# Performance work log

Hardware: AMD Instinct MI355X
Metric: run time of the kernel (lower is better)

Reference implementation:

```python
import jax, jax.numpy as jnp
import numpy as np

S, D, H = 2048, 1024, 16
DH = D // H
EPS = 1e-5


def setup_inputs() -> dict:
    key = jax.random.key(0)
    ks = jax.random.split(key, 6)
    scale = 0.02
    return {
        "inputs": jax.random.normal(ks[0], (S, D), dtype=jnp.float32),
        "ln_w": jnp.ones((D,), dtype=jnp.float32),
        "ln_b": jnp.zeros((D,), dtype=jnp.float32),
        "Wq": jax.random.normal(ks[1], (D, D), dtype=jnp.float32) * scale,
        "Wk": jax.random.normal(ks[2], (D, D), dtype=jnp.float32) * scale,
        "Wv": jax.random.normal(ks[3], (D, D), dtype=jnp.float32) * scale,
        "Wo": jax.random.normal(ks[4], (D, D), dtype=jnp.float32) * scale,
    }


def reference(inputs, ln_w, ln_b, Wq, Wk, Wv, Wo):
    # Pre-LayerNorm (per token), matching eqx.nn.LayerNorm (eps=1e-5)
    mu = jnp.mean(inputs, axis=-1, keepdims=True)
    var = jnp.var(inputs, axis=-1, keepdims=True)
    x = (inputs - mu) / jnp.sqrt(var + EPS) * ln_w + ln_b  # [S, D]

    # QKV projections (eqx Linear: y = W @ x, no bias) -> [S, H, DH]
    q = (x @ Wq.T).reshape(S, H, DH)
    k = (x @ Wk.T).reshape(S, H, DH)
    v = (x @ Wv.T).reshape(S, H, DH)

    # Scaled dot-product attention; softmax forced to full precision
    scores = jnp.einsum("shd,thd->hst", q, k) / jnp.sqrt(jnp.asarray(DH, x.dtype))
    attn = jax.nn.softmax(scores.astype(jnp.float32), axis=-1).astype(x.dtype)
    # (dropout is identity in inference mode)
    ctx = jnp.einsum("hst,thd->shd", attn, v).reshape(S, D)

    out = ctx @ Wo.T  # output projection
    # outer dropout is identity in inference mode; residual add
    return out + inputs
```

## Files before the change

### kernel.cpp

```cpp
#include <hip/hip_runtime.h>
#include <cstdint>
#include <cstddef>

typedef unsigned short u16;
typedef unsigned int u32;
typedef __attribute__((ext_vector_type(8))) short bf16x8;
typedef __attribute__((ext_vector_type(4))) short bf16x4;
typedef __attribute__((ext_vector_type(4))) float f32x4;
typedef __attribute__((ext_vector_type(4))) unsigned short u16x4;

#if __has_builtin(__builtin_amdgcn_mfma_f32_16x16x16bf16_1k)
#define MFMA16(a, b, c) __builtin_amdgcn_mfma_f32_16x16x16bf16_1k(a, b, c, 0, 0, 0)
#else
static __device__ __forceinline__ f32x4 mfma16_asm(bf16x4 a, bf16x4 b, f32x4 c) {
  asm volatile("v_mfma_f32_16x16x16_bf16 %0, %1, %2, %0\n\ts_nop 4"
               : "+v"(c) : "v"(a), "v"(b));
  return c;
}
#define MFMA16(a, b, c) mfma16_asm(a, b, c)
#endif

#if __has_builtin(__builtin_amdgcn_exp2f)
#define EXP2(x) __builtin_amdgcn_exp2f(x)
#else
#define EXP2(x) exp2f(x)
#endif

__device__ __forceinline__ u16 f2b(float f) {
  union { float f; unsigned u; } un; un.f = f;
  unsigned u = un.u;
  return (u16)((u + 0x7fffu + ((u >> 16) & 1u)) >> 16);
}

__device__ __forceinline__ u32 pkbf(float a, float b) {
  union { float f; u32 u; } ua, ub; ua.f = a; ub.f = b;
  return ((ua.u + 0x8000u) >> 16) | (((ub.u + 0x8000u) >> 16) << 16);
}

__device__ __forceinline__ void gload_lds16(const u16* g, u16* l) {
  __builtin_amdgcn_global_load_lds(
      (const __attribute__((address_space(1))) void*)g,
      (__attribute__((address_space(3))) void*)l, 16, 0, 0);
}

__device__ __forceinline__ void gemm128x128(
    const u16* __restrict__ A, const u16* __restrict__ B,
    u16* smA, u16* smB, int bm, int bn,
    float* outf, u16* outb, const float* __restrict__ resid, int ostride)
{
  const int tid = threadIdx.x;
  const int wave = tid >> 6, lane = tid & 63;
  const int quad = lane >> 4, l16 = lane & 15;
  const int wm = wave >> 1, wn = wave & 1;

  f32x4 acc[4][4];
  const f32x4 zero4 = {0.f, 0.f, 0.f, 0.f};
#pragma unroll
  for (int i = 0; i < 4; i++)
#pragma unroll
    for (int j = 0; j < 4; j++) acc[i][j] = zero4;

  const u16* Ab = A + (size_t)(bm * 128) * 1024;
  const u16* Bb = B + (size_t)(bn * 128) * 1024;

#define PSTAGE(buf, k0)                                                          \
  {                                                                              \
    _Pragma("unroll")                                                            \
    for (int i = 0; i < 4; i++) {                                                \
      const int idx = i * 256 + tid;                                             \
      const int row = idx >> 3, sl = idx & 7;                                    \
      const int g = (sl ^ (row & 7)) * 8;                                        \
      gload_lds16(Ab + (size_t)row * 1024 + (k0) + g,                            \
                  smA + (buf) * 8192 + (size_t)(i * 256 + wave * 64) * 8);       \
      gload_lds16(Bb + (size_t)row * 1024 + (k0) + g,                            \
                  smB + (buf) * 8192 + (size_t)(i * 256 + wave * 64) * 8);       \
    }                                                                            \
  }

  PSTAGE(0, 0);
  __syncthreads();
  for (int t = 0; t < 16; t++) {
    const int cur = t & 1;
    if (t < 15) PSTAGE(cur ^ 1, (t + 1) * 64);
    const u16* sa = smA + cur * 8192;
    const u16* sb = smB + cur * 8192;
#pragma unroll
    for (int ks = 0; ks < 2; ks++) {
      const int swz = ((ks * 4 + quad) ^ (l16 & 7)) * 8;
      bf16x8 afr[4], bfr[4];
#pragma unroll
      for (int mt = 0; mt < 4; mt++)
        afr[mt] = *(const bf16x8*)(sa + (wm * 64 + mt * 16 + l16) * 64 + swz);
#pragma unroll
      for (int nt = 0; nt < 4; nt++)
        bfr[nt] = *(const bf16x8*)(sb + (wn * 64 + nt * 16 + l16) * 64 + swz);
#pragma unroll
      for (int mt = 0; mt < 4; mt++)
#pragma unroll
        for (int nt = 0; nt < 4; nt++)
          acc[mt][nt] = __builtin_amdgcn_mfma_f32_16x16x32_bf16(afr[mt], bfr[nt], acc[mt][nt], 0, 0, 0);
    }
    __syncthreads();
  }
#undef PSTAGE

#pragma unroll
  for (int mt = 0; mt < 4; mt++)
#pragma unroll
    for (int nt = 0; nt < 4; nt++)
#pragma unroll
      for (int r = 0; r < 4; r++) {
        const int row = bm * 128 + wm * 64 + mt * 16 + quad * 4 + r;
        const int col = bn * 128 + wn * 64 + nt * 16 + l16;
        if (outb) outb[(size_t)row * ostride + col] = f2b(acc[mt][nt][r]);
        else outf[(size_t)row * ostride + col] =
                 acc[mt][nt][r] + resid[(size_t)row * ostride + col];
      }
}

__global__ __launch_bounds__(256, 2) void proj_k(
    const u16* __restrict__ xb, const u16* __restrict__ Wb,
    u16* __restrict__ qkbuf, u16* __restrict__ vTb)
{
  __shared__ u16 smA[2 * 128 * 64];
  __shared__ u16 smB[2 * 128 * 64];
  int b = blockIdx.x;
  const u16 *A, *B; u16* o; int bm, bn;
  if (b < 256) {
    const int c = b & 7, i = b >> 3;
    bm = ((c >> 2) << 3) | (i & 7);
    bn = ((c & 3) << 2) | (i >> 3);
    A = xb; B = Wb; o = qkbuf;
  } else {
    b -= 256;
    const int c = b & 7, i = b >> 3;
    bm = i & 7;
    bn = (c << 1) | (i >> 3);
    A = Wb + (size_t)2 * (1 << 20); B = xb; o = vTb;
  }
  gemm128x128(A, B, smA, smB, bm, bn, nullptr, o, nullptr, 2048);
}

__global__ __launch_bounds__(256, 2) void out_k(
    const u16* __restrict__ ctxb, const u16* __restrict__ Wob,
    float* __restrict__ out, const float* __restrict__ x)
{
  __shared__ u16 smA[2 * 128 * 64];
  __shared__ u16 smB[2 * 128 * 64];
  const int b = blockIdx.x;
  const int c = b & 7, i = b >> 3;
  const int bm = ((c >> 2) << 3) | (i & 7);
  const int bn = ((c & 3) << 1) | (i >> 3);
  gemm128x128(ctxb, Wob, smA, smB, bm, bn, out, nullptr, x, 1024);
}

__global__ __launch_bounds__(256) void pre_k(
    const float* __restrict__ x, const float* __restrict__ lnw, const float* __restrict__ lnb,
    const float* __restrict__ w0, const float* __restrict__ w1,
    const float* __restrict__ w2, const float* __restrict__ w3,
    u16* __restrict__ xb, u16* __restrict__ Wb)
{
  const int b = blockIdx.x;
  const int tid = threadIdx.x;
  if (b < 2048) {
    const int s = b;
    const float4 v = ((const float4*)(x + (size_t)s * 1024))[tid];
    float sum = v.x + v.y + v.z + v.w;
    float sq  = v.x * v.x + v.y * v.y + v.z * v.z + v.w * v.w;
#pragma unroll
    for (int off = 32; off >= 1; off >>= 1) {
      sum += __shfl_down(sum, off);
      sq  += __shfl_down(sq, off);
    }
    __shared__ float sS[4], sQ[4];
    const int wave = tid >> 6, lane = tid & 63;
    if (lane == 0) { sS[wave] = sum; sQ[wave] = sq; }
    __syncthreads();
    const float ts = sS[0] + sS[1] + sS[2] + sS[3];
    const float tq = sQ[0] + sQ[1] + sQ[2] + sQ[3];
    const float mu = ts * (1.0f / 1024.0f);
    const float var = tq * (1.0f / 1024.0f) - mu * mu;
    const float rstd = rsqrtf(var + 1e-5f);
    const float4 wv = ((const float4*)lnw)[tid];
    const float4 bv = ((const float4*)lnb)[tid];
    u16x4 o;
    o[0] = f2b((v.x - mu) * rstd * wv.x + bv.x);
    o[1] = f2b((v.y - mu) * rstd * wv.y + bv.y);
    o[2] = f2b((v.z - mu) * rstd * wv.z + bv.z);
    o[3] = f2b((v.w - mu) * rstd * wv.w + bv.w);
    *(u16x4*)(xb + (size_t)s * 1024 + tid * 4) = o;
  } else {
    const unsigned i = (unsigned)(b - 2048) * 1024u + tid * 4u;
    const unsigned NW = 1u << 20;
    const float* src; unsigned loc; float sc;
    if (i < NW)            { src = w0; loc = i;           sc = 0.18033688f; }
    else if (i < 2u * NW)  { src = w1; loc = i - NW;      sc = 1.0f; }
    else if (i < 3u * NW)  { src = w2; loc = i - 2u * NW; sc = 1.0f; }
    else                   { src = w3; loc = i - 3u * NW; sc = 1.0f; }
    const float4 v = *(const float4*)(src + loc);
    u16x4 r;
    r[0] = f2b(v.x * sc); r[1] = f2b(v.y * sc); r[2] = f2b(v.z * sc); r[3] = f2b(v.w * sc);
    *(u16x4*)(Wb + i) = r;
  }
}

__global__ __launch_bounds__(256, 2) void attn_k(
    const u16* __restrict__ qkbuf,
    const u16* __restrict__ vT,
    u16* __restrict__ ctx)
{
  const int bid = blockIdx.x;
  const int work = (bid & 7) * 64 + (bid >> 3);
  const int h = work >> 5;
  const int q0 = (work & 31) * 64;
  __shared__ __align__(16) unsigned char arena[65536];
  u16* kvbuf = (u16*)arena;
  const int tid = threadIdx.x;
  const int wave = tid >> 6, lane = tid & 63;
  const int quad = lane >> 4, l16 = lane & 15;
  const int a7 = l16 & 7;
  const u16* kg = qkbuf + 1024;

  bf16x8 qf[4][2];
#pragma unroll
  for (int s = 0; s < 4; s++)
#pragma unroll
    for (int ks = 0; ks < 2; ks++)
      qf[s][ks] = *(const bf16x8*)(qkbuf + (size_t)(q0 + s * 16 + l16) * 2048 + h * 64 + ks * 32 + quad * 8);

  const f32x4 zero4 = {0.f, 0.f, 0.f, 0.f};
  f32x4 Oacc[4][4];
#pragma unroll
  for (int s = 0; s < 4; s++)
#pragma unroll
    for (int dt = 0; dt < 4; dt++) Oacc[s][dt] = zero4;
  float lacc[4] = {0.f, 0.f, 0.f, 0.f};

#define STAGE(T, bf)                                                                     \
  {                                                                                      \
    _Pragma("unroll")                                                                    \
    for (int i = 0; i < 4; i++) {                                                        \
      const int idx = (wave * 4 + i) * 64 + lane;                                        \
      const int kt = idx >> 3, kc = (idx & 7) ^ (kt & 7);                                \
      gload_lds16(kg + (size_t)((T) * 128 + kt) * 2048 + h * 64 + kc * 8,                \
                  kvbuf + (bf) * 16384 + (size_t)(wave * 4 + i) * 512);                  \
      const int vd = idx >> 4, vc = (idx & 15) ^ (vd & 7);                               \
      gload_lds16(vT + (size_t)(h * 64 + vd) * 2048 + (T) * 128 + vc * 8,                \
                  kvbuf + (bf) * 16384 + 8192 + (size_t)(wave * 4 + i) * 512);           \
    }                                                                                    \
  }

  STAGE(0, 0);
  __syncthreads();

  for (int T = 0; T < 16; T++) {
    const int bf = T & 1;
    if (T + 1 < 16) STAGE(T + 1, 1 - bf);
    const u16* kb = kvbuf + bf * 16384;
    const u16* vb = kb + 8192;

    f32x4 st[2][4];
#pragma unroll
    for (int ntl = 0; ntl < 2; ntl++) {
      const int nt = wave * 2 + ntl;
      const u16* kr = kb + (nt * 16 + l16) * 64;
      const bf16x8 ka0 = *(const bf16x8*)(kr + (quad ^ a7) * 8);
      const bf16x8 ka1 = *(const bf16x8*)(kr + ((4 + quad) ^ a7) * 8);
#pragma unroll
      for (int s = 0; s < 4; s++) {
        f32x4 t0 = __builtin_amdgcn_mfma_f32_16x16x32_bf16(ka0, qf[s][0], zero4, 0, 0, 0);
        st[ntl][s] = __builtin_amdgcn_mfma_f32_16x16x32_bf16(ka1, qf[s][1], t0, 0, 0, 0);
      }
    }

    bf16x4 pk[2][4];
#pragma unroll
    for (int ntl = 0; ntl < 2; ntl++)
#pragma unroll
      for (int s = 0; s < 4; s++) {
        const float p0 = EXP2(st[ntl][s][0]);
        const float p1 = EXP2(st[ntl][s][1]);
        const float p2 = EXP2(st[ntl][s][2]);
        const float p3 = EXP2(st[ntl][s][3]);
        lacc[s] += (p0 + p1) + (p2 + p3);
        union { u32 u[2]; bf16x4 v; } pp;
        pp.u[0] = pkbf(p0, p1);
        pp.u[1] = pkbf(p2, p3);
        pk[ntl][s] = pp.v;
      }

#pragma unroll
    for (int ntl = 0; ntl < 2; ntl++)
#pragma unroll
      for (int dt = 0; dt < 4; dt++) {
        const bf16x4 bv = *(const bf16x4*)(vb + (dt * 16 + l16) * 128 +
            (((wave * 4 + ntl * 2 + (quad >> 1)) ^ a7) * 8 + (quad & 1) * 4));
#pragma unroll
        for (int s = 0; s < 4; s++)
          Oacc[s][dt] = MFMA16(pk[ntl][s], bv, Oacc[s][dt]);
      }
    __syncthreads();
  }
#undef STAGE

  float* rl = (float*)arena;
#pragma unroll
  for (int s = 0; s < 4; s++) {
    float l = lacc[s];
    l += __shfl_xor(l, 16);
    l += __shfl_xor(l, 32);
    if (quad == 0) rl[wave * 64 + s * 16 + l16] = l;
  }
  __syncthreads();
  const int m = tid >> 2, dg = (tid & 3) * 16;
  const float inv = 1.0f / (rl[m] + rl[64 + m] + rl[128 + m] + rl[192 + m]);
  __syncthreads();

  float* ro = (float*)arena;
#pragma unroll
  for (int s = 0; s < 4; s++)
#pragma unroll
    for (int dt = 0; dt < 4; dt++)
#pragma unroll
      for (int r = 0; r < 4; r++) {
        const int mr = s * 16 + quad * 4 + r;
        const int dc = (dt * 16 + l16) ^ ((mr & 7) << 1);
        ro[wave * 4096 + mr * 64 + dc] = Oacc[s][dt][r];
      }
  __syncthreads();
  u16* dst = ctx + (size_t)(q0 + m) * 1024 + h * 64 + dg;
  const int msw = (m & 7) << 1;
#pragma unroll
  for (int g = 0; g < 4; g++) {
    u16x4 o;
#pragma unroll
    for (int j = 0; j < 4; j++) {
      const int dc = (dg + g * 4 + j) ^ msw;
      const int base = m * 64 + dc;
      const float v = ro[base] + ro[4096 + base] + ro[8192 + base] + ro[12288 + base];
      o[j] = f2b(v * inv);
    }
    *(u16x4*)(dst + g * 4) = o;
  }
}

extern "C" void kernel_launch(void* const* d_in, const int* in_sizes, int n_in,
                              void* d_out, int out_size, void* d_ws, size_t ws_size,
                              hipStream_t stream)
{
  const float* x   = (const float*)d_in[0];
  const float* lnw = (const float*)d_in[1];
  const float* lnb = (const float*)d_in[2];
  const float* Wq  = (const float*)d_in[3];
  const float* Wk  = (const float*)d_in[4];
  const float* Wv  = (const float*)d_in[5];
  const float* Wo  = (const float*)d_in[6];

  u16* ws    = (u16*)d_ws;
  u16* xb    = ws;
  u16* Wb    = xb + (size_t)2048 * 1024;
  u16* qkbuf = Wb + (size_t)4 * 1024 * 1024;
  u16* vTb   = qkbuf + (size_t)2048 * 2048;
  u16* ctxb  = vTb + (size_t)1024 * 2048;

  pre_k<<<6144, 256, 0, stream>>>(x, lnw, lnb, Wq, Wk, Wv, Wo, xb, Wb);
  proj_k<<<384, 256, 0, stream>>>(xb, Wb, qkbuf, vTb);
  attn_k<<<512, 256, 0, stream>>>(qkbuf, vTb, ctxb);
  out_k<<<128, 256, 0, stream>>>(ctxb, Wb + (size_t)3 * (1 << 20), (float*)d_out, x);
}
```

Baseline: 150.8 us.

## Load K/V fragments directly from global memory and shrink LDS to raise occupancy

The attention kernel no longer double-buffers K and V tiles in LDS through async global-to-LDS loads with barriers each step. Each wave now reads its K and V MFMA fragments straight from global memory (relying on L2/cache), which removes the per-iteration __syncthreads. The epilogue reduction is split into two passes so LDS drops from 64KB to 32KB, and launch bounds rise to 3 blocks per CU. The cost is uncoalesced, repeated global loads with no software prefetch, so the MFMAs may stall on memory latency.

```diff
diff --git a/kernel.cpp b/kernel.cpp
--- a/kernel.cpp
+++ b/kernel.cpp
@@ -204,7 +204,7 @@
   }
 }
 
-__global__ __launch_bounds__(256, 2) void attn_k(
+__global__ __launch_bounds__(256, 3) void attn_k(
     const u16* __restrict__ qkbuf,
     const u16* __restrict__ vT,
     u16* __restrict__ ctx)
@@ -213,13 +213,10 @@
   const int work = (bid & 7) * 64 + (bid >> 3);
   const int h = work >> 5;
   const int q0 = (work & 31) * 64;
-  __shared__ __align__(16) unsigned char arena[65536];
-  u16* kvbuf = (u16*)arena;
+  __shared__ __align__(16) float arena[4 * 64 * 32];
   const int tid = threadIdx.x;
   const int wave = tid >> 6, lane = tid & 63;
   const int quad = lane >> 4, l16 = lane & 15;
-  const int a7 = l16 & 7;
-  const u16* kg = qkbuf + 1024;
 
   bf16x8 qf[4][2];
 #pragma unroll
@@ -236,36 +233,16 @@
     for (int dt = 0; dt < 4; dt++) Oacc[s][dt] = zero4;
   float lacc[4] = {0.f, 0.f, 0.f, 0.f};
 
-#define STAGE(T, bf)                                                                     \
-  {                                                                                      \
-    _Pragma("unroll")                                                                    \
-    for (int i = 0; i < 4; i++) {                                                        \
-      const int idx = (wave * 4 + i) * 64 + lane;                                        \
-      const int kt = idx >> 3, kc = (idx & 7) ^ (kt & 7);                                \
-      gload_lds16(kg + (size_t)((T) * 128 + kt) * 2048 + h * 64 + kc * 8,                \
-                  kvbuf + (bf) * 16384 + (size_t)(wave * 4 + i) * 512);                  \
-      const int vd = idx >> 4, vc = (idx & 15) ^ (vd & 7);                               \
-      gload_lds16(vT + (size_t)(h * 64 + vd) * 2048 + (T) * 128 + vc * 8,                \
-                  kvbuf + (bf) * 16384 + 8192 + (size_t)(wave * 4 + i) * 512);           \
-    }                                                                                    \
-  }
-
-  STAGE(0, 0);
-  __syncthreads();
+  const u16* kb = qkbuf + 1024 + h * 64 + (size_t)(wave * 32 + l16) * 2048;
+  const u16* vb = vT + (size_t)(h * 64 + l16) * 2048 + wave * 32;
 
   for (int T = 0; T < 16; T++) {
-    const int bf = T & 1;
-    if (T + 1 < 16) STAGE(T + 1, 1 - bf);
-    const u16* kb = kvbuf + bf * 16384;
-    const u16* vb = kb + 8192;
-
     f32x4 st[2][4];
 #pragma unroll
     for (int ntl = 0; ntl < 2; ntl++) {
-      const int nt = wave * 2 + ntl;
-      const u16* kr = kb + (nt * 16 + l16) * 64;
-      const bf16x8 ka0 = *(const bf16x8*)(kr + (quad ^ a7) * 8);
-      const bf16x8 ka1 = *(const bf16x8*)(kr + ((4 + quad) ^ a7) * 8);
+      const u16* kr = kb + (size_t)(T * 128 + ntl * 16) * 2048;
+      const bf16x8 ka0 = *(const bf16x8*)(kr + quad * 8);
+      const bf16x8 ka1 = *(const bf16x8*)(kr + 32 + quad * 8);
 #pragma unroll
       for (int s = 0; s < 4; s++) {
         f32x4 t0 = __builtin_amdgcn_mfma_f32_16x16x32_bf16(ka0, qf[s][0], zero4, 0, 0, 0);
@@ -293,17 +270,14 @@
     for (int ntl = 0; ntl < 2; ntl++)
 #pragma unroll
       for (int dt = 0; dt < 4; dt++) {
-        const bf16x4 bv = *(const bf16x4*)(vb + (dt * 16 + l16) * 128 +
-            (((wave * 4 + ntl * 2 + (quad >> 1)) ^ a7) * 8 + (quad & 1) * 4));
+        const bf16x4 bv = *(const bf16x4*)(vb + (size_t)(dt * 16) * 2048 + T * 128 + ntl * 16 + quad * 4);
 #pragma unroll
         for (int s = 0; s < 4; s++)
           Oacc[s][dt] = MFMA16(pk[ntl][s], bv, Oacc[s][dt]);
       }
-    __syncthreads();
-  }
-#undef STAGE
-
-  float* rl = (float*)arena;
+  }
+
+  float* rl = arena;
 #pragma unroll
   for (int s = 0; s < 4; s++) {
     float l = lacc[s];
@@ -312,35 +286,39 @@
     if (quad == 0) rl[wave * 64 + s * 16 + l16] = l;
   }
   __syncthreads();
-  const int m = tid >> 2, dg = (tid & 3) * 16;
+  const int m = tid >> 2;
+  const int c8 = (tid & 3) * 8;
   const float inv = 1.0f / (rl[m] + rl[64 + m] + rl[128 + m] + rl[192 + m]);
   __syncthreads();
 
-  float* ro = (float*)arena;
-#pragma unroll
-  for (int s = 0; s < 4; s++)
-#pragma unroll
-    for (int dt = 0; dt < 4; dt++)
-#pragma unroll
-      for (int r = 0; r < 4; r++) {
-        const int mr = s * 16 + quad * 4 + r;
-        const int dc = (dt * 16 + l16) ^ ((mr & 7) << 1);
-        ro[wave * 4096 + mr * 64 + dc] = Oacc[s][dt][r];
-      }
-  __syncthreads();
-  u16* dst = ctx + (size_t)(q0 + m) * 1024 + h * 64 + dg;
-  const int msw = (m & 7) << 1;
-#pragma unroll
-  for (int g = 0; g < 4; g++) {
-    u16x4 o;
-#pragma unroll
-    for (int j = 0; j < 4; j++) {
-      const int dc = (dg + g * 4 + j) ^ msw;
-      const int base = m * 64 + dc;
-      const float v = ro[base] + ro[4096 + base] + ro[8192 + base] + ro[12288 + base];
-      o[j] = f2b(v * inv);
+  float* ro = arena;
+  const int msw3 = (m & 3) << 3;
+#pragma unroll
+  for (int pass = 0; pass < 2; pass++) {
+#pragma unroll
+    for (int s = 0; s < 4; s++)
+#pragma unroll
+      for (int dtl = 0; dtl < 2; dtl++)
+#pragma unroll
+        for (int r = 0; r < 4; r++) {
+          const int mr = s * 16 + quad * 4 + r;
+          const int dc = (dtl * 16 + l16) ^ ((mr & 3) << 3);
+          ro[wave * 2048 + mr * 32 + dc] = Oacc[s][pass * 2 + dtl][r];
+        }
+    __syncthreads();
+    u16* dst = ctx + (size_t)(q0 + m) * 1024 + h * 64 + pass * 32 + c8;
+    float v[8];
+#pragma unroll
+    for (int j = 0; j < 8; j++) {
+      const int base = m * 32 + ((c8 + j) ^ msw3);
+      v[j] = ro[base] + ro[2048 + base] + ro[4096 + base] + ro[6144 + base];
     }
-    *(u16x4*)(dst + g * 4) = o;
+    u16x4 o0, o1;
+#pragma unroll
+    for (int j = 0; j < 4; j++) { o0[j] = f2b(v[j] * inv); o1[j] = f2b(v[4 + j] * inv); }
+    *(u16x4*)dst = o0;
+    *(u16x4*)(dst + 4) = o1;
+    __syncthreads();
   }
 }
 
```

Result: slower. 173.6 us (+15.1%).
